# Kernel tuning notes

Hardware: AMD Instinct MI355X
Metric: run time of the kernel (lower is better)

Reference implementation:

```python
import jax, jax.numpy as jnp
import numpy as np

N_NODES = 20000
N_USERS = 100000
N_PRODUCTS = 10000
D = 128
N_EDGES = 640000
N_LAYERS = 2


def gcn_conv(x, W, b, edge_index, num_nodes):
    """PyG-style GCNConv: add self-loops, symmetric degree norm, scatter-add."""
    h = x @ W  # [N, D]
    loop = jnp.arange(num_nodes, dtype=edge_index.dtype)
    src = jnp.concatenate([edge_index[0], loop])
    dst = jnp.concatenate([edge_index[1], loop])
    deg = jax.ops.segment_sum(jnp.ones_like(dst, dtype=h.dtype), dst,
                              num_segments=num_nodes)
    dinv = jnp.where(deg > 0, jax.lax.rsqrt(deg), 0.0)
    norm = dinv[src] * dinv[dst]  # [E+N]
    msg = norm[:, None] * h[src]  # gather + scale
    out = jax.ops.segment_sum(msg, dst, num_segments=num_nodes)  # scatter-add
    return out + b


def setup_inputs() -> dict:
    key = jax.random.key(0)
    ks = jax.random.split(key, 12)
    s = 0.05
    return {
        "user_ids": jax.random.randint(ks[0], (N_NODES,), 0, N_USERS),
        "product_ids": jax.random.randint(ks[1], (N_NODES,), 0, N_PRODUCTS),
        "edge_index_user": jax.random.randint(ks[2], (2, N_EDGES), 0, N_NODES),
        "edge_index_product": jax.random.randint(ks[3], (2, N_EDGES), 0, N_NODES),
        "user_emb_table": jax.random.normal(ks[4], (N_USERS, D), jnp.float32),
        "product_emb_table": jax.random.normal(ks[5], (N_PRODUCTS, D), jnp.float32),
        "user_conv_W": jax.random.normal(ks[6], (N_LAYERS, D, D), jnp.float32) * s,
        "user_conv_b": jnp.zeros((N_LAYERS, D), jnp.float32),
        "product_conv_W": jax.random.normal(ks[7], (N_LAYERS, D, D), jnp.float32) * s,
        "product_conv_b": jnp.zeros((N_LAYERS, D), jnp.float32),
        "out_W": jax.random.normal(ks[8], (2 * D, N_PRODUCTS), jnp.float32) * s,
        "out_b": jnp.zeros((N_PRODUCTS,), jnp.float32),
    }


def reference(user_ids, product_ids, edge_index_user, edge_index_product,
              user_emb_table, product_emb_table,
              user_conv_W, user_conv_b, product_conv_W, product_conv_b,
              out_W, out_b):
    u = user_emb_table[user_ids]       # [N, D]
    p = product_emb_table[product_ids]  # [N, D]
    for i in range(N_LAYERS):
        # dropout is identity in eval mode
        u = gcn_conv(u, user_conv_W[i], user_conv_b[i], edge_index_user, N_NODES)
        p = gcn_conv(p, product_conv_W[i], product_conv_b[i], edge_index_product, N_NODES)
    combined = jnp.concatenate([u, p], axis=1)  # [N, 2D]
    logits = combined @ out_W + out_b           # [N, n_products]
    return jax.nn.softmax(logits, axis=1)
```

## Files before the change

kernel.cpp:

```cpp
#include <hip/hip_runtime.h>
#include <cstdint>
#include <cstddef>

#define NN 20000
#define NE 640000
#define DD 128
#define NP 10000
#define NRT 1250
#define NRT_PAD 1256
#define NCT_PAD 632
#define NWG_BIG 474

typedef __attribute__((ext_vector_type(8))) short short8;
typedef __attribute__((ext_vector_type(4))) float f32x4;

static __device__ __forceinline__ unsigned short f2bf(float f){
  uint32_t u = __float_as_uint(f);
  return (unsigned short)((u + 0x7fffu + ((u >> 16) & 1u)) >> 16);
}
static __device__ __forceinline__ float bf2f(unsigned short u){
  return __uint_as_float(((uint32_t)u) << 16);
}

static __device__ __forceinline__ void gload_lds16(const void* g, void* l){
  __builtin_amdgcn_global_load_lds(
      (const __attribute__((address_space(1))) void*)g,
      (__attribute__((address_space(3))) void*)l, 16, 0, 0);
}

__global__ void k_count2(const int* __restrict__ dst_u, const int* __restrict__ dst_p,
                         int* __restrict__ cnt){
  int i = blockIdx.x * blockDim.x + threadIdx.x;
  if (i < NE) atomicAdd(&cnt[dst_u[i]], 1);
  else if (i < 2 * NE) atomicAdd(&cnt[NN + dst_p[i - NE]], 1);
}

__global__ void k_dinv2(const int* __restrict__ cnt, float* __restrict__ dinv){
  int i = blockIdx.x * blockDim.x + threadIdx.x;
  if (i < 2 * NN) dinv[i] = rsqrtf((float)(cnt[i] + 1));
}

__global__ void k_scan2(const int* __restrict__ cnt, int* __restrict__ row_off,
                        int* __restrict__ cursor){
  __shared__ int part[1024];
  const int g = blockIdx.x;
  const int* c = cnt + g * NN;
  int* ro = row_off + g * (NN + 1);
  int* cur = cursor + g * NN;
  int t = threadIdx.x;
  int per = (NN + 1023) >> 10;
  int base = t * per;
  int s = 0;
  for (int i = 0; i < per; i++){ int idx = base + i; if (idx < NN) s += c[idx]; }
  part[t] = s;
  __syncthreads();
  for (int off = 1; off < 1024; off <<= 1){
    int v = (t >= off) ? part[t - off] : 0;
    __syncthreads();
    part[t] += v;
    __syncthreads();
  }
  int run = (t == 0) ? 0 : part[t - 1];
  for (int i = 0; i < per; i++){
    int idx = base + i;
    if (idx < NN){ ro[idx] = run; cur[idx] = run; run += c[idx]; }
  }
  if (t == 0) ro[NN] = part[1023];
}

__global__ void k_fill2(const int* __restrict__ src_u, const int* __restrict__ dst_u,
                        const int* __restrict__ src_p, const int* __restrict__ dst_p,
                        int* __restrict__ cursor, int* __restrict__ col){
  int i = blockIdx.x * blockDim.x + threadIdx.x;
  if (i < NE){
    int p = atomicAdd(&cursor[dst_u[i]], 1);
    col[p] = src_u[i];
  } else if (i < 2 * NE){
    int j = i - NE;
    int p = atomicAdd(&cursor[NN + dst_p[j]], 1);
    col[NE + p] = src_p[j];
  }
}


__global__ void k_gather2(const float* __restrict__ utab, const int* __restrict__ uids,
                          const float* __restrict__ ptab, const int* __restrict__ pids,
                          unsigned short* __restrict__ xu, unsigned short* __restrict__ xp){
  const float* tab = blockIdx.y ? ptab : utab;
  const int*   ids = blockIdx.y ? pids : uids;
  unsigned short* xf = blockIdx.y ? xp : xu;
  int node = blockIdx.x * blockDim.y + threadIdx.y;
  int tx = threadIdx.x;
  if (node >= NN) return;
  const float4 v = *reinterpret_cast<const float4*>(tab + (size_t)ids[node] * DD + tx * 4);
  ushort4 o; o.x = f2bf(v.x); o.y = f2bf(v.y); o.z = f2bf(v.z); o.w = f2bf(v.w);
  size_t chunk = ((size_t)(node >> 4) * 4 + (tx >> 3)) * 64 + ((tx >> 1) & 3) * 16 + (node & 15);
  *reinterpret_cast<ushort4*>(xf + chunk * 8 + (tx & 1) * 4) = o;
}

__global__ void k_wfrag4(const float* __restrict__ uW, const float* __restrict__ pW,
                         unsigned short* __restrict__ WuF0, unsigned short* __restrict__ WuF1,
                         unsigned short* __restrict__ WpF0, unsigned short* __restrict__ WpF1){
  const float* W; unsigned short* Wf;
  switch (blockIdx.y){
    case 0: W = uW;                    Wf = WuF0; break;
    case 1: W = uW + (size_t)DD * DD;  Wf = WuF1; break;
    case 2: W = pW;                    Wf = WpF0; break;
    default:W = pW + (size_t)DD * DD;  Wf = WpF1; break;
  }
  int i = blockIdx.x * blockDim.x + threadIdx.x;
  if (i >= DD * DD) return;
  int e = i & 7, l = (i >> 3) & 63, rem = i >> 9;
  int kt = rem & 3, ct = rem >> 2;
  int col = ct * 16 + (l & 15);
  int k = kt * 32 + (l >> 4) * 8 + e;
  Wf[i] = f2bf(W[(size_t)k * DD + col]);
}

__global__ __launch_bounds__(256) void k_wfrag2(const float* __restrict__ W,
                                                unsigned short* __restrict__ Wf){
  __shared__ float tile[32][33];
  const int kb = blockIdx.y * 32, cb = blockIdx.x * 32;
  const int tx = threadIdx.x & 31, ty = threadIdx.x >> 5;
  const int col = cb + tx;
  #pragma unroll
  for (int j = 0; j < 4; j++){
    int k = ty + j * 8;
    tile[k][tx] = (col < NP) ? W[(size_t)(kb + k) * NP + col] : 0.f;
  }
  __syncthreads();
  const int t = threadIdx.x;
  const int ct2 = t >> 7, rep = t & 1, l = (t >> 1) & 63;
  const int c_loc = ct2 * 16 + (l & 15);
  const int k_loc = (l >> 4) * 8 + rep * 4;
  ushort4 o;
  o.x = f2bf(tile[k_loc + 0][c_loc]);
  o.y = f2bf(tile[k_loc + 1][c_loc]);
  o.z = f2bf(tile[k_loc + 2][c_loc]);
  o.w = f2bf(tile[k_loc + 3][c_loc]);
  const int ct = cb / 16 + ct2, kt = kb / 32;
  *reinterpret_cast<ushort4*>(Wf + ((size_t)(ct * 8 + kt) * 64 + l) * 8 + rep * 4) = o;
}

__global__ __launch_bounds__(256) void k_conv2(
        const unsigned short* __restrict__ Au, const unsigned short* __restrict__ Ap,
        const unsigned short* __restrict__ Wu, const unsigned short* __restrict__ Wp,
        const float* __restrict__ du, const float* __restrict__ dp,
        unsigned short* __restrict__ hu, unsigned short* __restrict__ hp){
  const unsigned short* Af = blockIdx.y ? Ap : Au;
  const unsigned short* Wf = blockIdx.y ? Wp : Wu;
  const float* dinv        = blockIdx.y ? dp : du;
  unsigned short* hsb      = blockIdx.y ? hp : hu;
  int gw = blockIdx.x * 4 + (threadIdx.x >> 6);
  int lane = threadIdx.x & 63;
  bool valid = gw < NRT;
  int R = valid ? gw : (NRT - 1);
  short8 a[4];
  #pragma unroll
  for (int kt = 0; kt < 4; kt++)
    a[kt] = *reinterpret_cast<const short8*>(Af + ((size_t)(R * 4 + kt) * 64 + lane) * 8);
  int fr = lane & 15, fq = lane >> 4;
  #pragma unroll
  for (int ct = 0; ct < 8; ct++){
    f32x4 acc = {0.f, 0.f, 0.f, 0.f};
    #pragma unroll
    for (int kt = 0; kt < 4; kt++){
      short8 b = *reinterpret_cast<const short8*>(Wf + ((size_t)(ct * 4 + kt) * 64 + lane) * 8);
      acc = __builtin_amdgcn_mfma_f32_16x16x32_bf16(a[kt], b, acc, 0, 0, 0);
    }
    if (valid){
      #pragma unroll
      for (int r = 0; r < 4; r++){
        int grow = R * 16 + fq * 4 + r;
        hsb[(size_t)grow * DD + ct * 16 + fr] = f2bf(dinv[grow] * acc[r]);
      }
    }
  }
}

__global__ void k_agg2(const unsigned short* __restrict__ hu, const unsigned short* __restrict__ hp,
                       const float* __restrict__ du, const float* __restrict__ dp,
                       const int* __restrict__ ro, const int* __restrict__ colb,
                       const float* __restrict__ bu, const float* __restrict__ bp,
                       unsigned short* __restrict__ xfu, unsigned short* __restrict__ xfp,
                       int KT, int toff_p){
  const int g = blockIdx.y;
  const unsigned short* hsb = g ? hp : hu;
  const float* dinv = g ? (dp + NN) - NN : du;
  const float* dv   = g ? dp : du;
  const float* bias = g ? bp : bu;
  unsigned short* xf = g ? xfp : xfu;
  const int* row_off = ro + g * (NN + 1);
  const int* col     = colb + (size_t)g * NE;
  const int toff = g ? toff_p : 0;
  (void)dinv;

  int node = blockIdx.x * blockDim.y + threadIdx.y;
  int tx = threadIdx.x;
  if (node >= NN) return;
  const short8* h8 = reinterpret_cast<const short8*>(hsb);
  float a[8];
  {
    short8 v = h8[(size_t)node * 16 + tx];
    #pragma unroll
    for (int j = 0; j < 8; j++) a[j] = bf2f((unsigned short)v[j]);
  }
  int s = row_off[node], e = row_off[node + 1];
  int i = s;
  for (; i + 1 < e; i += 2){
    short8 v0 = h8[(size_t)col[i] * 16 + tx];
    short8 v1 = h8[(size_t)col[i + 1] * 16 + tx];
    #pragma unroll
    for (int j = 0; j < 8; j++) a[j] += bf2f((unsigned short)v0[j]) + bf2f((unsigned short)v1[j]);
  }
  if (i < e){
    short8 v = h8[(size_t)col[i] * 16 + tx];
    #pragma unroll
    for (int j = 0; j < 8; j++) a[j] += bf2f((unsigned short)v[j]);
  }
  float dn = dv[node];
  short8 ov;
  #pragma unroll
  for (int j = 0; j < 8; j++)
    ov[j] = (short)f2bf(dn * a[j] + bias[tx * 8 + j]);
  size_t chunk = ((size_t)(node >> 4) * KT + toff + (tx >> 2)) * 64 + (tx & 3) * 16 + (node & 15);
  *reinterpret_cast<short8*>(xf + chunk * 8) = ov;
}

template<int PASS>
__global__ __launch_bounds__(256, 2) void k_big(
    const unsigned short* __restrict__ Af, const unsigned short* __restrict__ Bf,
    const float* __restrict__ ob, float* __restrict__ rowsum, float* __restrict__ out){
  __shared__ unsigned short sA[2][16384];
  const int tid = threadIdx.x, lane = tid & 63, wid = tid >> 6;
  const int wm = wid >> 1, wn = wid & 1;
  const int fr = lane & 15, fq = lane >> 4;

  const int orig = blockIdx.x;
  const int xcd = orig & 7, pos = orig >> 3;
  const int wgid = (xcd < 2 ? xcd * 60 : 120 + (xcd - 2) * 59) + pos;
  const int cp = wgid / 6, six = wgid - cp * 6;
  const int rt0 = six * 52 + (six < 2 ? six : 2);
  const int nrt = 52 + (six < 2 ? 1 : 0);
  const int bct = cp * 8;

  short8 breg[4][8];
  #pragma unroll
  for (int n = 0; n < 4; n++)
    #pragma unroll
    for (int kt = 0; kt < 8; kt++)
      breg[n][kt] = *reinterpret_cast<const short8*>(
          Bf + (((size_t)(bct + wn * 4 + n) * 8 + kt) * 64 + lane) * 8);

  float obv[4];
  #pragma unroll
  for (int n = 0; n < 4; n++){
    int gcol = cp * 128 + wn * 64 + n * 16 + fr;
    obv[n] = (gcol < NP) ? ob[gcol] : 0.f;
  }

#define STAGEA(buf, rt) do{                                                    \
    _Pragma("unroll")                                                          \
    for (int i_ = 0; i_ < 8; i_++){                                            \
      int c_ = i_ * 256 + tid;                                                 \
      gload_lds16(Af + ((size_t)(rt) * 2048 + c_) * 8, (void*)&sA[buf][c_ * 8]); \
    } }while(0)

  STAGEA(0, rt0);
  for (int t = 0; t < nrt; t++){
    const int p = t & 1;
    if (t + 1 < nrt){
      STAGEA(p ^ 1, rt0 + t + 1);
      asm volatile("s_waitcnt vmcnt(8)" ::: "memory");
    } else {
      asm volatile("s_waitcnt vmcnt(0)" ::: "memory");
    }
    __builtin_amdgcn_s_barrier();

    f32x4 acc[2][4] = {};
    #pragma unroll
    for (int m = 0; m < 2; m++)
      #pragma unroll
      for (int kt = 0; kt < 8; kt++){
        short8 a = *reinterpret_cast<const short8*>(
            &sA[p][(((wm * 2 + m) * 8 + kt) * 64 + lane) * 8]);
        #pragma unroll
        for (int n = 0; n < 4; n++)
          acc[m][n] = __builtin_amdgcn_mfma_f32_16x16x32_bf16(a, breg[n][kt], acc[m][n], 0, 0, 0);
      }
    __builtin_amdgcn_s_barrier();

    const int rbase = (rt0 + t) * 64 + wm * 32;
    if (PASS == 0){
      #pragma unroll
      for (int m = 0; m < 2; m++)
        #pragma unroll
        for (int r = 0; r < 4; r++){
          const int grow = rbase + m * 16 + fq * 4 + r;
          float rs = 0.f;
          #pragma unroll
          for (int n = 0; n < 4; n++){
            const int gcol = cp * 128 + wn * 64 + n * 16 + fr;
            rs += (gcol < NP) ? __expf(acc[m][n][r] + obv[n]) : 0.f;
          }
          rs += __shfl_xor(rs, 1, 64);
          rs += __shfl_xor(rs, 2, 64);
          rs += __shfl_xor(rs, 4, 64);
          rs += __shfl_xor(rs, 8, 64);
          if (fr == 0 && grow < NN) atomicAdd(&rowsum[grow], rs);
        }
    } else {
      #pragma unroll
      for (int m = 0; m < 2; m++)
        #pragma unroll
        for (int r = 0; r < 4; r++){
          const int grow = rbase + m * 16 + fq * 4 + r;
          const bool rv = grow < NN;
          const float ri = rv ? 1.f / rowsum[grow] : 0.f;
          #pragma unroll
          for (int n = 0; n < 4; n++){
            const int gcol = cp * 128 + wn * 64 + n * 16 + fr;
            if (rv && gcol < NP)
              __builtin_nontemporal_store(ri * __expf(acc[m][n][r] + obv[n]),
                                          &out[(size_t)grow * NP + gcol]);
          }
        }
    }
  }
#undef STAGEA
}

extern "C" void kernel_launch(void* const* d_in, const int* in_sizes, int n_in,
                              void* d_out, int out_size, void* d_ws, size_t ws_size,
                              hipStream_t stream){
  const int*   user_ids = (const int*)d_in[0];
  const int*   prod_ids = (const int*)d_in[1];
  const int*   ei_u     = (const int*)d_in[2];
  const int*   ei_p     = (const int*)d_in[3];
  const float* utab     = (const float*)d_in[4];
  const float* ptab     = (const float*)d_in[5];
  const float* uW       = (const float*)d_in[6];
  const float* ub       = (const float*)d_in[7];
  const float* pW       = (const float*)d_in[8];
  const float* pb       = (const float*)d_in[9];
  const float* oW       = (const float*)d_in[10];
  const float* ob       = (const float*)d_in[11];
  float* out = (float*)d_out;
  (void)in_sizes; (void)n_in; (void)out_size; (void)ws_size;

  char* w = (char*)d_ws;
  size_t off = 0;
  auto alloc = [&](size_t bytes)->void*{
    void* p = w + off; off += (bytes + 255) & ~(size_t)255; return p;
  };
  int*   cnt    = (int*)alloc(2 * NN * 4);
  float* rowsum = (float*)alloc(NN * 4);
  float* dinv   = (float*)alloc(2 * NN * 4);
  int*   ro     = (int*)alloc(2 * (NN + 1) * 4);
  int*   cur    = (int*)alloc(2 * NN * 4);
  int*   colb   = (int*)alloc((size_t)2 * NE * 4);
  unsigned short* xu_f  = (unsigned short*)alloc((size_t)NN * DD * 2);
  unsigned short* xp_f  = (unsigned short*)alloc((size_t)NN * DD * 2);
  unsigned short* xu2_f = (unsigned short*)alloc((size_t)NN * DD * 2);
  unsigned short* xp2_f = (unsigned short*)alloc((size_t)NN * DD * 2);
  unsigned short* comb_f= (unsigned short*)alloc((size_t)NRT_PAD * 8 * 64 * 8 * 2);
  unsigned short* hu    = (unsigned short*)alloc((size_t)NN * DD * 2);
  unsigned short* hp    = (unsigned short*)alloc((size_t)NN * DD * 2);
  unsigned short* WuF0 = (unsigned short*)alloc((size_t)DD * DD * 2);
  unsigned short* WuF1 = (unsigned short*)alloc((size_t)DD * DD * 2);
  unsigned short* WpF0 = (unsigned short*)alloc((size_t)DD * DD * 2);
  unsigned short* WpF1 = (unsigned short*)alloc((size_t)DD * DD * 2);
  unsigned short* WoF  = (unsigned short*)alloc((size_t)NCT_PAD * 8 * 64 * 8 * 2);

  hipMemsetAsync(cnt, 0, (2 * NN + NN) * 4, stream);
  hipMemsetAsync(comb_f + (size_t)NRT * 8 * 64 * 8, 0,
                 (size_t)(NRT_PAD - NRT) * 8 * 64 * 8 * 2, stream);

  const int* src_u = ei_u;  const int* dst_u = ei_u + NE;
  const int* src_p = ei_p;  const int* dst_p = ei_p + NE;

  k_count2<<<(2 * NE + 255) / 256, 256, 0, stream>>>(dst_u, dst_p, cnt);
  k_dinv2<<<(2 * NN + 255) / 256, 256, 0, stream>>>(cnt, dinv);
  k_scan2<<<2, 1024, 0, stream>>>(cnt, ro, cur);
  k_fill2<<<(2 * NE + 255) / 256, 256, 0, stream>>>(src_u, dst_u, src_p, dst_p, cur, colb);

  dim3 gblk(32, 8);
  k_gather2<<<dim3(NN / 8, 2), gblk, 0, stream>>>(utab, user_ids, ptab, prod_ids, xu_f, xp_f);

  k_wfrag4<<<dim3(64, 4), 256, 0, stream>>>(uW, pW, WuF0, WuF1, WpF0, WpF1);
  k_wfrag2<<<dim3(316, 8), 256, 0, stream>>>(oW, WoF);

  const int convGrid = (NRT + 3) / 4;
  dim3 aggBlk(16, 16);
  const int aggGrid = (NN + 15) / 16;

  k_conv2<<<dim3(convGrid, 2), 256, 0, stream>>>(xu_f, xp_f, WuF0, WpF0,
                                                 dinv, dinv + NN, hu, hp);
  k_agg2<<<dim3(aggGrid, 2), aggBlk, 0, stream>>>(hu, hp, dinv, dinv + NN, ro, colb,
                                                  ub, pb, xu2_f, xp2_f, 4, 0);
  k_conv2<<<dim3(convGrid, 2), 256, 0, stream>>>(xu2_f, xp2_f, WuF1, WpF1,
                                                 dinv, dinv + NN, hu, hp);
  k_agg2<<<dim3(aggGrid, 2), aggBlk, 0, stream>>>(hu, hp, dinv, dinv + NN, ro, colb,
                                                  ub + DD, pb + DD, comb_f, comb_f, 8, 4);

  k_big<0><<<NWG_BIG, 256, 0, stream>>>(comb_f, WoF, ob, rowsum, out);
  k_big<1><<<NWG_BIG, 256, 0, stream>>>(comb_f, WoF, ob, rowsum, out);
}
```

Before: 723.0 us.

## Merge preprocessing kernels into one launch and deepen aggregation unroll

Combines degree counting, embedding gather, conv-weight fragmenting and output-weight fragmenting into one block-partitioned prep kernel, and folds the rsqrt degree normalisation into the scan kernel. This removes several small kernel launches and their serialisation gaps. The aggregation loop now gathers four neighbour rows per iteration instead of two, which gives more memory-level parallelism. The big GEMM raises wave priority around its MFMA block. In exchange the prep kernel runs unrelated work in one grid with a shared LDS tile, and the wider unroll raises register use.

```diff
diff --git a/kernel.cpp b/kernel.cpp
--- a/kernel.cpp
+++ b/kernel.cpp
@@ -28,30 +28,99 @@
       (__attribute__((address_space(3))) void*)l, 16, 0, 0);
 }
 
-__global__ void k_count2(const int* __restrict__ dst_u, const int* __restrict__ dst_p,
-                         int* __restrict__ cnt){
-  int i = blockIdx.x * blockDim.x + threadIdx.x;
-  if (i < NE) atomicAdd(&cnt[dst_u[i]], 1);
-  else if (i < 2 * NE) atomicAdd(&cnt[NN + dst_p[i - NE]], 1);
-}
-
-__global__ void k_dinv2(const int* __restrict__ cnt, float* __restrict__ dinv){
-  int i = blockIdx.x * blockDim.x + threadIdx.x;
-  if (i < 2 * NN) dinv[i] = rsqrtf((float)(cnt[i] + 1));
+#define PREP_NWG 12784
+__global__ __launch_bounds__(256) void k_prep(
+    const int* __restrict__ dst_u, const int* __restrict__ dst_p, int* __restrict__ cnt,
+    const float* __restrict__ utab, const int* __restrict__ uids,
+    const float* __restrict__ ptab, const int* __restrict__ pids,
+    unsigned short* __restrict__ xu, unsigned short* __restrict__ xp,
+    const float* __restrict__ uW, const float* __restrict__ pW,
+    unsigned short* __restrict__ WuF0, unsigned short* __restrict__ WuF1,
+    unsigned short* __restrict__ WpF0, unsigned short* __restrict__ WpF1,
+    const float* __restrict__ oW, unsigned short* __restrict__ WoF){
+  __shared__ float tile[32][33];
+  const int b = blockIdx.x, tid = threadIdx.x;
+
+  if (b < 5000){
+    int i = b * 256 + tid;
+    if (i < NE) atomicAdd(&cnt[dst_u[i]], 1);
+    else atomicAdd(&cnt[NN + dst_p[i - NE]], 1);
+
+  } else if (b < 10000){
+    int bg = b - 5000;
+    int tower = bg / 2500, nb = bg % 2500;
+    const float* tab = tower ? ptab : utab;
+    const int*   ids = tower ? pids : uids;
+    unsigned short* xf = tower ? xp : xu;
+    int tx = tid & 31, ny = tid >> 5;
+    int node = nb * 8 + ny;
+    const float4 v = *reinterpret_cast<const float4*>(tab + (size_t)ids[node] * DD + tx * 4);
+    ushort4 o; o.x = f2bf(v.x); o.y = f2bf(v.y); o.z = f2bf(v.z); o.w = f2bf(v.w);
+    size_t chunk = ((size_t)(node >> 4) * 4 + (tx >> 3)) * 64 + ((tx >> 1) & 3) * 16 + (node & 15);
+    *reinterpret_cast<ushort4*>(xf + chunk * 8 + (tx & 1) * 4) = o;
+
+  } else if (b < 10256){
+    int bw = b - 10000;
+    int wy = bw >> 6, bx = bw & 63;
+    const float* W; unsigned short* Wf;
+    switch (wy){
+      case 0: W = uW;                   Wf = WuF0; break;
+      case 1: W = uW + (size_t)DD * DD; Wf = WuF1; break;
+      case 2: W = pW;                   Wf = WpF0; break;
+      default:W = pW + (size_t)DD * DD; Wf = WpF1; break;
+    }
+    int i = bx * 256 + tid;
+    int e = i & 7, l = (i >> 3) & 63, rem = i >> 9;
+    int kt = rem & 3, ct = rem >> 2;
+    int col = ct * 16 + (l & 15);
+    int k = kt * 32 + (l >> 4) * 8 + e;
+    Wf[i] = f2bf(W[(size_t)k * DD + col]);
+
+  } else {
+    int bw = b - 10256;
+    int bx = bw % 316, by = bw / 316;
+    const int kb = by * 32, cb = bx * 32;
+    const int tx = tid & 31, ty = tid >> 5;
+    const int col = cb + tx;
+    #pragma unroll
+    for (int j = 0; j < 4; j++){
+      int k = ty + j * 8;
+      tile[k][tx] = (col < NP) ? oW[(size_t)(kb + k) * NP + col] : 0.f;
+    }
+    __syncthreads();
+    const int ct2 = tid >> 7, rep = tid & 1, l = (tid >> 1) & 63;
+    const int c_loc = ct2 * 16 + (l & 15);
+    const int k_loc = (l >> 4) * 8 + rep * 4;
+    ushort4 o;
+    o.x = f2bf(tile[k_loc + 0][c_loc]);
+    o.y = f2bf(tile[k_loc + 1][c_loc]);
+    o.z = f2bf(tile[k_loc + 2][c_loc]);
+    o.w = f2bf(tile[k_loc + 3][c_loc]);
+    const int ct = cb / 16 + ct2, kt = kb / 32;
+    *reinterpret_cast<ushort4*>(WoF + ((size_t)(ct * 8 + kt) * 64 + l) * 8 + rep * 4) = o;
+  }
 }
 
 __global__ void k_scan2(const int* __restrict__ cnt, int* __restrict__ row_off,
-                        int* __restrict__ cursor){
+                        int* __restrict__ cursor, float* __restrict__ dinv){
   __shared__ int part[1024];
   const int g = blockIdx.x;
   const int* c = cnt + g * NN;
   int* ro = row_off + g * (NN + 1);
   int* cur = cursor + g * NN;
+  float* dv = dinv + g * NN;
   int t = threadIdx.x;
   int per = (NN + 1023) >> 10;
   int base = t * per;
   int s = 0;
-  for (int i = 0; i < per; i++){ int idx = base + i; if (idx < NN) s += c[idx]; }
+  for (int i = 0; i < per; i++){
+    int idx = base + i;
+    if (idx < NN){
+      int cv = c[idx];
+      dv[idx] = rsqrtf((float)(cv + 1));
+      s += cv;
+    }
+  }
   part[t] = s;
   __syncthreads();
   for (int off = 1; off < 1024; off <<= 1){
@@ -80,66 +149,6 @@
     int p = atomicAdd(&cursor[NN + dst_p[j]], 1);
     col[NE + p] = src_p[j];
   }
-}
-
-
-__global__ void k_gather2(const float* __restrict__ utab, const int* __restrict__ uids,
-                          const float* __restrict__ ptab, const int* __restrict__ pids,
-                          unsigned short* __restrict__ xu, unsigned short* __restrict__ xp){
-  const float* tab = blockIdx.y ? ptab : utab;
-  const int*   ids = blockIdx.y ? pids : uids;
-  unsigned short* xf = blockIdx.y ? xp : xu;
-  int node = blockIdx.x * blockDim.y + threadIdx.y;
-  int tx = threadIdx.x;
-  if (node >= NN) return;
-  const float4 v = *reinterpret_cast<const float4*>(tab + (size_t)ids[node] * DD + tx * 4);
-  ushort4 o; o.x = f2bf(v.x); o.y = f2bf(v.y); o.z = f2bf(v.z); o.w = f2bf(v.w);
-  size_t chunk = ((size_t)(node >> 4) * 4 + (tx >> 3)) * 64 + ((tx >> 1) & 3) * 16 + (node & 15);
-  *reinterpret_cast<ushort4*>(xf + chunk * 8 + (tx & 1) * 4) = o;
-}
-
-__global__ void k_wfrag4(const float* __restrict__ uW, const float* __restrict__ pW,
-                         unsigned short* __restrict__ WuF0, unsigned short* __restrict__ WuF1,
-                         unsigned short* __restrict__ WpF0, unsigned short* __restrict__ WpF1){
-  const float* W; unsigned short* Wf;
-  switch (blockIdx.y){
-    case 0: W = uW;                    Wf = WuF0; break;
-    case 1: W = uW + (size_t)DD * DD;  Wf = WuF1; break;
-    case 2: W = pW;                    Wf = WpF0; break;
-    default:W = pW + (size_t)DD * DD;  Wf = WpF1; break;
-  }
-  int i = blockIdx.x * blockDim.x + threadIdx.x;
-  if (i >= DD * DD) return;
-  int e = i & 7, l = (i >> 3) & 63, rem = i >> 9;
-  int kt = rem & 3, ct = rem >> 2;
-  int col = ct * 16 + (l & 15);
-  int k = kt * 32 + (l >> 4) * 8 + e;
-  Wf[i] = f2bf(W[(size_t)k * DD + col]);
-}
-
-__global__ __launch_bounds__(256) void k_wfrag2(const float* __restrict__ W,
-                                                unsigned short* __restrict__ Wf){
-  __shared__ float tile[32][33];
-  const int kb = blockIdx.y * 32, cb = blockIdx.x * 32;
-  const int tx = threadIdx.x & 31, ty = threadIdx.x >> 5;
-  const int col = cb + tx;
-  #pragma unroll
-  for (int j = 0; j < 4; j++){
-    int k = ty + j * 8;
-    tile[k][tx] = (col < NP) ? W[(size_t)(kb + k) * NP + col] : 0.f;
-  }
-  __syncthreads();
-  const int t = threadIdx.x;
-  const int ct2 = t >> 7, rep = t & 1, l = (t >> 1) & 63;
-  const int c_loc = ct2 * 16 + (l & 15);
-  const int k_loc = (l >> 4) * 8 + rep * 4;
-  ushort4 o;
-  o.x = f2bf(tile[k_loc + 0][c_loc]);
-  o.y = f2bf(tile[k_loc + 1][c_loc]);
-  o.z = f2bf(tile[k_loc + 2][c_loc]);
-  o.w = f2bf(tile[k_loc + 3][c_loc]);
-  const int ct = cb / 16 + ct2, kt = kb / 32;
-  *reinterpret_cast<ushort4*>(Wf + ((size_t)(ct * 8 + kt) * 64 + l) * 8 + rep * 4) = o;
 }
 
 __global__ __launch_bounds__(256) void k_conv2(
@@ -186,14 +195,12 @@
                        int KT, int toff_p){
   const int g = blockIdx.y;
   const unsigned short* hsb = g ? hp : hu;
-  const float* dinv = g ? (dp + NN) - NN : du;
   const float* dv   = g ? dp : du;
   const float* bias = g ? bp : bu;
   unsigned short* xf = g ? xfp : xfu;
   const int* row_off = ro + g * (NN + 1);
   const int* col     = colb + (size_t)g * NE;
   const int toff = g ? toff_p : 0;
-  (void)dinv;
 
   int node = blockIdx.x * blockDim.y + threadIdx.y;
   int tx = threadIdx.x;
@@ -207,13 +214,17 @@
   }
   int s = row_off[node], e = row_off[node + 1];
   int i = s;
-  for (; i + 1 < e; i += 2){
+  for (; i + 3 < e; i += 4){
     short8 v0 = h8[(size_t)col[i] * 16 + tx];
     short8 v1 = h8[(size_t)col[i + 1] * 16 + tx];
-    #pragma unroll
-    for (int j = 0; j < 8; j++) a[j] += bf2f((unsigned short)v0[j]) + bf2f((unsigned short)v1[j]);
-  }
-  if (i < e){
+    short8 v2 = h8[(size_t)col[i + 2] * 16 + tx];
+    short8 v3 = h8[(size_t)col[i + 3] * 16 + tx];
+    #pragma unroll
+    for (int j = 0; j < 8; j++)
+      a[j] += (bf2f((unsigned short)v0[j]) + bf2f((unsigned short)v1[j]))
+            + (bf2f((unsigned short)v2[j]) + bf2f((unsigned short)v3[j]));
+  }
+  for (; i < e; i++){
     short8 v = h8[(size_t)col[i] * 16 + tx];
     #pragma unroll
     for (int j = 0; j < 8; j++) a[j] += bf2f((unsigned short)v[j]);
@@ -278,6 +289,7 @@
     __builtin_amdgcn_s_barrier();
 
     f32x4 acc[2][4] = {};
+    __builtin_amdgcn_s_setprio(1);
     #pragma unroll
     for (int m = 0; m < 2; m++)
       #pragma unroll
@@ -288,6 +300,7 @@
         for (int n = 0; n < 4; n++)
           acc[m][n] = __builtin_amdgcn_mfma_f32_16x16x32_bf16(a, breg[n][kt], acc[m][n], 0, 0, 0);
       }
+    __builtin_amdgcn_s_setprio(0);
     __builtin_amdgcn_s_barrier();
 
     const int rbase = (rt0 + t) * 64 + wm * 32;
@@ -379,16 +392,11 @@
   const int* src_u = ei_u;  const int* dst_u = ei_u + NE;
   const int* src_p = ei_p;  const int* dst_p = ei_p + NE;
 
-  k_count2<<<(2 * NE + 255) / 256, 256, 0, stream>>>(dst_u, dst_p, cnt);
-  k_dinv2<<<(2 * NN + 255) / 256, 256, 0, stream>>>(cnt, dinv);
-  k_scan2<<<2, 1024, 0, stream>>>(cnt, ro, cur);
+  k_prep<<<PREP_NWG, 256, 0, stream>>>(dst_u, dst_p, cnt,
+                                       utab, user_ids, ptab, prod_ids, xu_f, xp_f,
+                                       uW, pW, WuF0, WuF1, WpF0, WpF1, oW, WoF);
+  k_scan2<<<2, 1024, 0, stream>>>(cnt, ro, cur, dinv);
   k_fill2<<<(2 * NE + 255) / 256, 256, 0, stream>>>(src_u, dst_u, src_p, dst_p, cur, colb);
-
-  dim3 gblk(32, 8);
-  k_gather2<<<dim3(NN / 8, 2), gblk, 0, stream>>>(utab, user_ids, ptab, prod_ids, xu_f, xp_f);
-
-  k_wfrag4<<<dim3(64, 4), 256, 0, stream>>>(uW, pW, WuF0, WuF1, WpF0, WpF1);
-  k_wfrag2<<<dim3(316, 8), 256, 0, stream>>>(oW, WoF);
 
   const int convGrid = (NRT + 3) / 4;
   dim3 aggBlk(16, 16);
```

Result: faster. 704.0 us (median of 2 runs) (-2.6%).
